# Optimization experiments

Hardware: AMD Instinct MI355X
Metric: run time of the kernel (lower is better)

The kernel has to match this reference:

```python
import jax, jax.numpy as jnp
import numpy as np

N, E = 50000, 800000          # nodes, edges
D_EMB, D_HID = 64, 64          # n_embed, n_hidden


def setup_inputs() -> dict:
    key = jax.random.key(0)
    k0, k1, k2, k3 = jax.random.split(key, 4)
    prop_edge_index = jax.random.randint(k0, (2, E), 0, N, dtype=jnp.int32)
    emb = jax.random.normal(k1, (N, D_EMB), dtype=jnp.float32)          # embedding.weight
    W1 = jax.random.normal(k2, (D_EMB, D_HID), dtype=jnp.float32) / np.float32(np.sqrt(D_EMB))
    b1 = jnp.zeros((D_HID,), jnp.float32)
    W2 = jax.random.normal(k3, (D_HID, D_HID), dtype=jnp.float32) / np.float32(np.sqrt(D_HID))
    b2 = jnp.zeros((D_HID,), jnp.float32)
    return {"prop_edge_index": prop_edge_index, "emb": emb,
            "W1": W1, "b1": b1, "W2": W2, "b2": b2}


def _gcn_conv(x, W, b, src, dst, n):
    """PyG GCNConv: D^{-1/2}(A+I)D^{-1/2} (x @ W) + b, aggregation at dst."""
    h = x @ W                                                   # [N, D]
    deg = jax.ops.segment_sum(jnp.ones_like(dst, jnp.float32), dst,
                              num_segments=n) + 1.0             # +1 self-loop
    dinv = jax.lax.rsqrt(deg)                                   # [N]
    coef = dinv[src] * dinv[dst]                                # [E]
    msg = h[src] * coef[:, None]                                # [E, D] gather
    agg = jax.ops.segment_sum(msg, dst, num_segments=n)         # scatter-add
    agg = agg + h * (dinv * dinv)[:, None]                      # self-loop term
    return agg + b


def reference(prop_edge_index, emb, W1, b1, W2, b2):
    src, dst = prop_edge_index[0], prop_edge_index[1]
    x = jax.nn.relu(_gcn_conv(emb, W1, b1, src, dst, N))
    # dropout is identity at inference (args.training = False)
    return _gcn_conv(x, W2, b2, src, dst, N)
```

## Files before the change

kernel.cpp:

```cpp
#include <hip/hip_runtime.h>
#include <hip/hip_fp16.h>

#define D 64
#define KMAX 64

__global__ __launch_bounds__(256) void k_zero(int* __restrict__ p, int n4) {
    int stride = gridDim.x * blockDim.x;
    for (int i = blockIdx.x * blockDim.x + threadIdx.x; i < n4; i += stride)
        reinterpret_cast<int4*>(p)[i] = make_int4(0, 0, 0, 0);
}

__global__ __launch_bounds__(256) void k_fill_gemm(
    const int* __restrict__ src, const int* __restrict__ dst,
    int* __restrict__ cnt, int* __restrict__ csr, int e, int n,
    const float* __restrict__ X, const float* __restrict__ W,
    __half* __restrict__ G, int ntiles, int fill_blocks) {
    __shared__ float Ws[D][D];
    __shared__ float Xs[16][D + 4];

    if (blockIdx.x < fill_blocks) {
        int r = blockIdx.x & 7;
        int lo = (int)(((long long)r * n) >> 3);
        int hi = (int)(((long long)(r + 1) * n) >> 3);
        int nch = fill_blocks >> 3;
        int chunk = blockIdx.x >> 3;
        for (int i = chunk * blockDim.x + threadIdx.x; i < e; i += nch * blockDim.x) {
            int d = dst[i];
            if (d >= lo && d < hi) {
                int pos = atomicAdd(&cnt[d], 1);
                csr[(d << 6) + pos] = src[i];
            }
        }
        return;
    }

    int tid = threadIdx.x;
    int rl = tid >> 4;
    int c4 = tid & 15;
    int gb = blockIdx.x - fill_blocks;
    int ngb = gridDim.x - fill_blocks;

    for (int i = tid; i < (D * D) / 4; i += 256)
        reinterpret_cast<float4*>(&Ws[0][0])[i] = reinterpret_cast<const float4*>(W)[i];

    for (int tile = gb; tile < ntiles; tile += ngb) {
        int row = tile * 16 + rl;
        __syncthreads();
        {
            float4 v = make_float4(0.f, 0.f, 0.f, 0.f);
            if (row < n) v = reinterpret_cast<const float4*>(X)[(size_t)row * 16 + c4];
            *reinterpret_cast<float4*>(&Xs[rl][c4 * 4]) = v;
        }
        __syncthreads();

        float4 acc = make_float4(0.f, 0.f, 0.f, 0.f);
#pragma unroll
        for (int k = 0; k < D; ++k) {
            float xk = Xs[rl][k];
            float4 w = *reinterpret_cast<const float4*>(&Ws[k][c4 * 4]);
            acc.x += xk * w.x; acc.y += xk * w.y;
            acc.z += xk * w.z; acc.w += xk * w.w;
        }
        if (row < n) {
            __half2 h01 = __floats2half2_rn(acc.x, acc.y);
            __half2 h23 = __floats2half2_rn(acc.z, acc.w);
            int2 packed;
            packed.x = *reinterpret_cast<int*>(&h01);
            packed.y = *reinterpret_cast<int*>(&h23);
            reinterpret_cast<int2*>(G)[(size_t)row * 16 + c4] = packed;
        }
    }
}

template <bool RELU>
__global__ __launch_bounds__(256) void k_agg(const __half* __restrict__ G,
                                             const int* __restrict__ cnt,
                                             const int* __restrict__ csr,
                                             const float* __restrict__ bias,
                                             float* __restrict__ out, int n) {
    int wid = (blockIdx.x * blockDim.x + threadIdx.x) >> 6;
    if (wid >= n) return;
    int lane = threadIdx.x & 63;
    int eq = lane >> 4;
    int c4 = lane & 15;
    int deg = cnt[wid];
    int beg = wid << 6;
    int end = beg + deg;

    float4 acc = make_float4(0.f, 0.f, 0.f, 0.f);
    for (int e = beg + eq; e < end; e += 4) {
        int s = __builtin_nontemporal_load(&csr[e]);
        float ds = rsqrtf((float)(cnt[s] + 1));
        int2 raw = reinterpret_cast<const int2*>(G)[(size_t)s * 16 + c4];
        __half2 p0 = *reinterpret_cast<__half2*>(&raw.x);
        __half2 p1 = *reinterpret_cast<__half2*>(&raw.y);
        float2 f0 = __half22float2(p0);
        float2 f1 = __half22float2(p1);
        acc.x += ds * f0.x; acc.y += ds * f0.y;
        acc.z += ds * f1.x; acc.w += ds * f1.y;
    }
#pragma unroll
    for (int off = 16; off < 64; off <<= 1) {
        acc.x += __shfl_xor(acc.x, off);
        acc.y += __shfl_xor(acc.y, off);
        acc.z += __shfl_xor(acc.z, off);
        acc.w += __shfl_xor(acc.w, off);
    }
    if (eq == 0) {
        float dv = rsqrtf((float)(deg + 1));
        int2 raw = reinterpret_cast<const int2*>(G)[(size_t)wid * 16 + c4];
        __half2 p0 = *reinterpret_cast<__half2*>(&raw.x);
        __half2 p1 = *reinterpret_cast<__half2*>(&raw.y);
        float2 f0 = __half22float2(p0);
        float2 f1 = __half22float2(p1);
        float4 b4 = reinterpret_cast<const float4*>(bias)[c4];
        float4 o;
        o.x = (acc.x + dv * f0.x) * dv + b4.x;
        o.y = (acc.y + dv * f0.y) * dv + b4.y;
        o.z = (acc.z + dv * f1.x) * dv + b4.z;
        o.w = (acc.w + dv * f1.y) * dv + b4.w;
        if (RELU) {
            o.x = fmaxf(o.x, 0.f); o.y = fmaxf(o.y, 0.f);
            o.z = fmaxf(o.z, 0.f); o.w = fmaxf(o.w, 0.f);
        }
        reinterpret_cast<float4*>(out)[(size_t)wid * 16 + c4] = o;
    }
}

__global__ __launch_bounds__(256, 4) void k_gemm2b(const float* __restrict__ X,
                                                   const float* __restrict__ W,
                                                   __half* __restrict__ G, int n, int ntiles) {
    __shared__ float Ws[D][D];
    __shared__ float Xs[32][D];
    int tid = threadIdx.x;
    int col = tid & 63;
    int rq = tid >> 6;

    for (int i = tid; i < (D * D) / 4; i += 256)
        reinterpret_cast<float4*>(&Ws[0][0])[i] = reinterpret_cast<const float4*>(W)[i];

    for (int tile = blockIdx.x; tile < ntiles; tile += gridDim.x) {
        int rowbase = tile * 32;
        __syncthreads();
        if (rowbase + 32 <= n) {
            const float4* xp = reinterpret_cast<const float4*>(X + (size_t)rowbase * D);
            for (int i = tid; i < (32 * D) / 4; i += 256)
                reinterpret_cast<float4*>(&Xs[0][0])[i] = xp[i];
        } else {
            for (int i = tid; i < 32 * D; i += 256) {
                int r = rowbase + (i >> 6);
                Xs[i >> 6][i & 63] = (r < n) ? X[(size_t)r * D + (i & 63)] : 0.f;
            }
        }
        __syncthreads();

        float acc[8];
#pragma unroll
        for (int j = 0; j < 8; ++j) acc[j] = 0.f;
#pragma unroll 4
        for (int k4 = 0; k4 < D; k4 += 4) {
            float w0 = Ws[k4 + 0][col];
            float w1 = Ws[k4 + 1][col];
            float w2 = Ws[k4 + 2][col];
            float w3 = Ws[k4 + 3][col];
#pragma unroll
            for (int j = 0; j < 8; ++j) {
                float4 xv = *reinterpret_cast<const float4*>(&Xs[(rq << 3) + j][k4]);
                acc[j] += xv.x * w0 + xv.y * w1 + xv.z * w2 + xv.w * w3;
            }
        }
#pragma unroll
        for (int j = 0; j < 8; ++j) {
            int r = rowbase + (rq << 3) + j;
            if (r < n) G[(size_t)r * D + col] = __float2half(acc[j]);
        }
    }
}


extern "C" void kernel_launch(void* const* d_in, const int* in_sizes, int n_in,
                              void* d_out, int out_size, void* d_ws, size_t ws_size,
                              hipStream_t stream) {
    const int* ei = (const int*)d_in[0];
    const float* emb = (const float*)d_in[1];
    const float* W1 = (const float*)d_in[2];
    const float* b1 = (const float*)d_in[3];
    const float* W2 = (const float*)d_in[4];
    const float* b2 = (const float*)d_in[5];
    float* out = (float*)d_out;

    int E = in_sizes[0] / 2;
    int N = in_sizes[1] / D;
    const int* src = ei;
    const int* dst = ei + E;

    auto al = [](size_t v) { return (v + 255) & ~(size_t)255; };
    char* ws = (char*)d_ws;
    size_t off = 0;
    int* cnt = (int*)(ws + off);      off = al(off + (size_t)N * 4);
    int* csr = (int*)(ws + off);      off = al(off + (size_t)N * KMAX * 4);
    __half* g1 = (__half*)(ws + off); off = al(off + (size_t)N * D * 2);
    float* x = (float*)(ws + off);    off = al(off + (size_t)N * D * 4);
    __half* g2 = (__half*)(ws + off); off = al(off + (size_t)N * D * 2);

    int ntiles16 = (N + 15) / 16;
    int ntiles32 = (N + 31) / 32;
    int fill_blocks = 1024;
    int gemm_blocks = 1024;
    int row_blocks = (N + 3) / 4;

    hipLaunchKernelGGL(k_zero, dim3(512), dim3(256), 0, stream, cnt, (N + 3) / 4);
    hipLaunchKernelGGL(k_fill_gemm, dim3(fill_blocks + gemm_blocks), dim3(256), 0, stream,
                       src, dst, cnt, csr, E, N, emb, W1, g1, ntiles16, fill_blocks);
    hipLaunchKernelGGL(k_agg<true>, dim3(row_blocks), dim3(256), 0, stream,
                       g1, cnt, csr, b1, x, N);
    hipLaunchKernelGGL(k_gemm2b, dim3(1024), dim3(256), 0, stream,
                       x, W2, g2, N, ntiles32);
    hipLaunchKernelGGL(k_agg<false>, dim3(row_blocks), dim3(256), 0, stream,
                       g2, cnt, csr, b2, out, N);
}
```

Before: 140.2 us.

## Fuse first-layer aggregation with second GEMM via shared-memory tile

```diff
diff --git a/kernel.cpp b/kernel.cpp
--- a/kernel.cpp
+++ b/kernel.cpp
@@ -72,12 +72,96 @@
     }
 }
 
-template <bool RELU>
-__global__ __launch_bounds__(256) void k_agg(const __half* __restrict__ G,
-                                             const int* __restrict__ cnt,
-                                             const int* __restrict__ csr,
-                                             const float* __restrict__ bias,
-                                             float* __restrict__ out, int n) {
+__global__ __launch_bounds__(256, 4) void k_agg_gemm2(
+    const __half* __restrict__ G1, const int* __restrict__ cnt,
+    const int* __restrict__ csr, const float* __restrict__ b1,
+    const float* __restrict__ W2, __half* __restrict__ G2, int n, int ntiles) {
+    __shared__ float Ws[D][D];
+    __shared__ float xs[32][D];
+    int tid = threadIdx.x;
+    int wv = tid >> 6;
+    int lane = tid & 63;
+    int eq = lane >> 4;
+    int c4 = lane & 15;
+
+    for (int i = tid; i < (D * D) / 4; i += 256)
+        reinterpret_cast<float4*>(&Ws[0][0])[i] = reinterpret_cast<const float4*>(W2)[i];
+
+    for (int tile = blockIdx.x; tile < ntiles; tile += gridDim.x) {
+        int rowbase = tile * 32;
+
+        for (int j = 0; j < 8; ++j) {
+            int wid = rowbase + (wv << 3) + j;
+            float4 o = make_float4(0.f, 0.f, 0.f, 0.f);
+            if (wid < n) {
+                int deg = cnt[wid];
+                int beg = wid << 6;
+                int end = beg + deg;
+                float4 acc = make_float4(0.f, 0.f, 0.f, 0.f);
+                for (int e = beg + eq; e < end; e += 4) {
+                    int s = __builtin_nontemporal_load(&csr[e]);
+                    float ds = rsqrtf((float)(cnt[s] + 1));
+                    int2 raw = reinterpret_cast<const int2*>(G1)[(size_t)s * 16 + c4];
+                    __half2 p0 = *reinterpret_cast<__half2*>(&raw.x);
+                    __half2 p1 = *reinterpret_cast<__half2*>(&raw.y);
+                    float2 f0 = __half22float2(p0);
+                    float2 f1 = __half22float2(p1);
+                    acc.x += ds * f0.x; acc.y += ds * f0.y;
+                    acc.z += ds * f1.x; acc.w += ds * f1.y;
+                }
+#pragma unroll
+                for (int off = 16; off < 64; off <<= 1) {
+                    acc.x += __shfl_xor(acc.x, off);
+                    acc.y += __shfl_xor(acc.y, off);
+                    acc.z += __shfl_xor(acc.z, off);
+                    acc.w += __shfl_xor(acc.w, off);
+                }
+                float dv = rsqrtf((float)(deg + 1));
+                int2 raw = reinterpret_cast<const int2*>(G1)[(size_t)wid * 16 + c4];
+                __half2 p0 = *reinterpret_cast<__half2*>(&raw.x);
+                __half2 p1 = *reinterpret_cast<__half2*>(&raw.y);
+                float2 f0 = __half22float2(p0);
+                float2 f1 = __half22float2(p1);
+                float4 b4 = reinterpret_cast<const float4*>(b1)[c4];
+                o.x = fmaxf((acc.x + dv * f0.x) * dv + b4.x, 0.f);
+                o.y = fmaxf((acc.y + dv * f0.y) * dv + b4.y, 0.f);
+                o.z = fmaxf((acc.z + dv * f1.x) * dv + b4.z, 0.f);
+                o.w = fmaxf((acc.w + dv * f1.y) * dv + b4.w, 0.f);
+            }
+            if (eq == 0) *reinterpret_cast<float4*>(&xs[(wv << 3) + j][c4 * 4]) = o;
+        }
+
+        __syncthreads();
+
+        float acc[8];
+#pragma unroll
+        for (int j = 0; j < 8; ++j) acc[j] = 0.f;
+#pragma unroll 4
+        for (int k4 = 0; k4 < D; k4 += 4) {
+            float w0 = Ws[k4 + 0][lane];
+            float w1 = Ws[k4 + 1][lane];
+            float w2 = Ws[k4 + 2][lane];
+            float w3 = Ws[k4 + 3][lane];
+#pragma unroll
+            for (int j = 0; j < 8; ++j) {
+                float4 xv = *reinterpret_cast<const float4*>(&xs[(wv << 3) + j][k4]);
+                acc[j] += xv.x * w0 + xv.y * w1 + xv.z * w2 + xv.w * w3;
+            }
+        }
+#pragma unroll
+        for (int j = 0; j < 8; ++j) {
+            int r = rowbase + (wv << 3) + j;
+            if (r < n) G2[(size_t)r * D + lane] = __float2half(acc[j]);
+        }
+        __syncthreads();
+    }
+}
+
+__global__ __launch_bounds__(256) void k_agg2(const __half* __restrict__ G,
+                                              const int* __restrict__ cnt,
+                                              const int* __restrict__ csr,
+                                              const float* __restrict__ bias,
+                                              float* __restrict__ out, int n) {
     int wid = (blockIdx.x * blockDim.x + threadIdx.x) >> 6;
     if (wid >= n) return;
     int lane = threadIdx.x & 63;
@@ -119,61 +203,7 @@
         o.y = (acc.y + dv * f0.y) * dv + b4.y;
         o.z = (acc.z + dv * f1.x) * dv + b4.z;
         o.w = (acc.w + dv * f1.y) * dv + b4.w;
-        if (RELU) {
-            o.x = fmaxf(o.x, 0.f); o.y = fmaxf(o.y, 0.f);
-            o.z = fmaxf(o.z, 0.f); o.w = fmaxf(o.w, 0.f);
-        }
         reinterpret_cast<float4*>(out)[(size_t)wid * 16 + c4] = o;
-    }
-}
-
-__global__ __launch_bounds__(256, 4) void k_gemm2b(const float* __restrict__ X,
-                                                   const float* __restrict__ W,
-                                                   __half* __restrict__ G, int n, int ntiles) {
-    __shared__ float Ws[D][D];
-    __shared__ float Xs[32][D];
-    int tid = threadIdx.x;
-    int col = tid & 63;
-    int rq = tid >> 6;
-
-    for (int i = tid; i < (D * D) / 4; i += 256)
-        reinterpret_cast<float4*>(&Ws[0][0])[i] = reinterpret_cast<const float4*>(W)[i];
-
-    for (int tile = blockIdx.x; tile < ntiles; tile += gridDim.x) {
-        int rowbase = tile * 32;
-        __syncthreads();
-        if (rowbase + 32 <= n) {
-            const float4* xp = reinterpret_cast<const float4*>(X + (size_t)rowbase * D);
-            for (int i = tid; i < (32 * D) / 4; i += 256)
-                reinterpret_cast<float4*>(&Xs[0][0])[i] = xp[i];
-        } else {
-            for (int i = tid; i < 32 * D; i += 256) {
-                int r = rowbase + (i >> 6);
-                Xs[i >> 6][i & 63] = (r < n) ? X[(size_t)r * D + (i & 63)] : 0.f;
-            }
-        }
-        __syncthreads();
-
-        float acc[8];
-#pragma unroll
-        for (int j = 0; j < 8; ++j) acc[j] = 0.f;
-#pragma unroll 4
-        for (int k4 = 0; k4 < D; k4 += 4) {
-            float w0 = Ws[k4 + 0][col];
-            float w1 = Ws[k4 + 1][col];
-            float w2 = Ws[k4 + 2][col];
-            float w3 = Ws[k4 + 3][col];
-#pragma unroll
-            for (int j = 0; j < 8; ++j) {
-                float4 xv = *reinterpret_cast<const float4*>(&Xs[(rq << 3) + j][k4]);
-                acc[j] += xv.x * w0 + xv.y * w1 + xv.z * w2 + xv.w * w3;
-            }
-        }
-#pragma unroll
-        for (int j = 0; j < 8; ++j) {
-            int r = rowbase + (rq << 3) + j;
-            if (r < n) G[(size_t)r * D + col] = __float2half(acc[j]);
-        }
     }
 }
 
@@ -200,7 +230,6 @@
     int* cnt = (int*)(ws + off);      off = al(off + (size_t)N * 4);
     int* csr = (int*)(ws + off);      off = al(off + (size_t)N * KMAX * 4);
     __half* g1 = (__half*)(ws + off); off = al(off + (size_t)N * D * 2);
-    float* x = (float*)(ws + off);    off = al(off + (size_t)N * D * 4);
     __half* g2 = (__half*)(ws + off); off = al(off + (size_t)N * D * 2);
 
     int ntiles16 = (N + 15) / 16;
@@ -212,10 +241,8 @@
     hipLaunchKernelGGL(k_zero, dim3(512), dim3(256), 0, stream, cnt, (N + 3) / 4);
     hipLaunchKernelGGL(k_fill_gemm, dim3(fill_blocks + gemm_blocks), dim3(256), 0, stream,
                        src, dst, cnt, csr, E, N, emb, W1, g1, ntiles16, fill_blocks);
-    hipLaunchKernelGGL(k_agg<true>, dim3(row_blocks), dim3(256), 0, stream,
-                       g1, cnt, csr, b1, x, N);
-    hipLaunchKernelGGL(k_gemm2b, dim3(1024), dim3(256), 0, stream,
-                       x, W2, g2, N, ntiles32);
-    hipLaunchKernelGGL(k_agg<false>, dim3(row_blocks), dim3(256), 0, stream,
+    hipLaunchKernelGGL(k_agg_gemm2, dim3(1024), dim3(256), 0, stream,
+                       g1, cnt, csr, b1, W2, g2, N, ntiles32);
+    hipLaunchKernelGGL(k_agg2, dim3(row_blocks), dim3(256), 0, stream,
                        g2, cnt, csr, b2, out, N);
 }
```

After: 167.7 us. +19.6%, slower.
